# Optimization experiments

Measured on AMD Instinct MI355X. Metric: run time of the kernel, lower is better.

The kernel has to match this reference:

```python
import jax, jax.numpy as jnp
import numpy as np

B, S, F, U = 64, 512, 128, 512          # seq_length == units (required for broadcast in original code)
SIGDIM = F + F * F                       # level-2 truncated signature dimension
GRID_SIZE, SPLINE_ORDER = 5, 3           # efficient-KAN style defaults
NB = GRID_SIZE + SPLINE_ORDER            # number of b-spline basis functions per input feature
LN_EPS = 1e-3                            # keras LayerNormalization default epsilon


def _make_grid():
    h = 2.0 / GRID_SIZE  # uniform grid on [-1, 1], extended by spline order
    return -1.0 + h * jnp.arange(-SPLINE_ORDER, GRID_SIZE + SPLINE_ORDER + 1, dtype=jnp.float32)


def _b_splines(x, grid):
    # x: (N, F) -> (N, F, NB) via Cox-de Boor recursion
    x = x[..., None]
    bases = ((x >= grid[:-1]) & (x < grid[1:])).astype(x.dtype)
    for p in range(1, SPLINE_ORDER + 1):
        left = (x - grid[:-(p + 1)]) / (grid[p:-1] - grid[:-(p + 1)])
        right = (grid[p + 1:] - x) / (grid[p + 1:] - grid[1:-p])
        bases = left * bases[..., :-1] + right * bases[..., 1:]
    return bases


def _kan_linear(x, base_w, spline_w, grid):
    # KANLinear, no bias / no layernorm: silu base branch + b-spline branch
    lead = x.shape[:-1]
    base = jax.nn.silu(x) @ base_w                                  # (..., U)
    b = _b_splines(x.reshape(-1, x.shape[-1]), grid)                # (N, F, NB)
    spl = jnp.einsum('nfk,ufk->nu', b, spline_w).reshape(*lead, base_w.shape[1])
    return base + spl


def _signature2(x):
    # level-2 path signature of piecewise-linear path x: (B, S, F) -> (B, F + F*F)
    dx = x[:, 1:] - x[:, :-1]                                       # (B, S-1, F)
    s1 = dx.sum(axis=1)                                             # (B, F)
    cs = jnp.cumsum(dx, axis=1)
    prev = jnp.concatenate([jnp.zeros_like(cs[:, :1]), cs[:, :-1]], axis=1)
    s2 = jnp.einsum('bti,btj->bij', prev + 0.5 * dx, dx)            # (B, F, F)
    return jnp.concatenate([s1, s2.reshape(x.shape[0], -1)], axis=-1)


def _grkan(sig, w1, b1, w2, b2, w3, b3, w4, b4, ws, bs, gamma, beta):
    # gated residual network mapping signature -> softmax attention weights (B, U)
    h = jax.nn.elu(sig @ w1 + b1)
    h = h @ w2 + b2
    glu = jax.nn.sigmoid(h @ w3 + b3) * (h @ w4 + b4)
    y = sig @ ws + bs + glu
    mu = jnp.mean(y, axis=-1, keepdims=True)
    var = jnp.var(y, axis=-1, keepdims=True)
    y = (y - mu) / jnp.sqrt(var + LN_EPS) * gamma + beta
    return jax.nn.softmax(y, axis=-1)


def setup_inputs() -> dict:
    key = jax.random.key(0)
    ks = jax.random.split(key, 24)
    n = lambda k, shp, s=0.02: jax.random.normal(k, shp, dtype=jnp.float32) * s
    inp = {
        'inputs': jax.random.normal(ks[0], (B, S, F), dtype=jnp.float32),
        'h_prev': jax.random.normal(ks[1], (B, U), dtype=jnp.float32),
        'c_prev': jax.random.normal(ks[2], (B, U), dtype=jnp.float32),
        'time_kernel': n(ks[3], (S, 1), 0.1),
        'kan_base_w': n(ks[4], (F, U)),
        'kan_spline_w': n(ks[5], (U, F, NB)),
        'g_w1': n(ks[6], (SIGDIM, U)), 'g_b1': jnp.zeros((U,), jnp.float32),
        'g_w2': n(ks[7], (U, U)), 'g_b2': jnp.zeros((U,), jnp.float32),
        'g_w3': n(ks[8], (U, U)), 'g_b3': jnp.zeros((U,), jnp.float32),
        'g_w4': n(ks[9], (U, U)), 'g_b4': jnp.zeros((U,), jnp.float32),
        'g_skip_w': n(ks[10], (SIGDIM, U)), 'g_skip_b': jnp.zeros((U,), jnp.float32),
        'ln_gamma': jnp.ones((U,), jnp.float32), 'ln_beta': jnp.zeros((U,), jnp.float32),
        'wf': n(ks[11], (2 * U, U)), 'bf': jnp.zeros((U,), jnp.float32),
        'wi': n(ks[12], (2 * U, U)), 'bi': jnp.zeros((U,), jnp.float32),
        'wc': n(ks[13], (2 * U, U)), 'bc': jnp.zeros((U,), jnp.float32),
        'wo': n(ks[14], (2 * U, U)), 'bo': jnp.zeros((U,), jnp.float32),
    }
    return inp


def reference(inputs, h_prev, c_prev, time_kernel, kan_base_w, kan_spline_w,
              g_w1, g_b1, g_w2, g_b2, g_w3, g_b3, g_w4, g_b4, g_skip_w, g_skip_b,
              ln_gamma, ln_beta, wf, bf, wi, bi, wc, bc, wo, bo):
    grid = _make_grid()
    weighted = time_kernel * inputs                                  # (B,S,F)
    sig = _signature2(weighted)                                      # (B,SIGDIM)
    attn = _grkan(sig, g_w1, g_b1, g_w2, g_b2, g_w3, g_b3, g_w4, g_b4,
                  g_skip_w, g_skip_b, ln_gamma, ln_beta)             # (B,S) since U==S
    kan_out = _kan_linear(weighted, kan_base_w, kan_spline_w, grid)  # (B,S,U)
    attended = kan_out * attn[..., None]                             # (B,S,U)
    current = attended.mean(axis=1)                                  # (B,U)
    combined = jnp.concatenate([current, h_prev], axis=-1)           # (B,2U)
    f = jax.nn.sigmoid(combined @ wf + bf)
    i = jax.nn.sigmoid(combined @ wi + bi)
    cand = jnp.tanh(combined @ wc + bc)
    o = jax.nn.sigmoid(combined @ wo + bo)
    c_new = f * c_prev + i * cand
    h_new = o * jnp.tanh(c_new)
    return h_new, c_new
```

## Files before the change

kernel.cpp:

```cpp
#include <hip/hip_runtime.h>
#include <math.h>

#define BB 64
#define SS 512
#define FF 128
#define UU 512
#define NBB 8
#define SIGDIM (FF + FF*FF)
#define K3 16512
#define KK 1152
#define SIG_KC 43
#define SIG_STEPS 6

typedef __attribute__((ext_vector_type(8))) __bf16 bf16x8;
typedef __attribute__((ext_vector_type(8))) unsigned short u16x8;
typedef __attribute__((ext_vector_type(4))) float f32x4;

__device__ __forceinline__ unsigned short f2bf(float x) {
    unsigned int u = __float_as_uint(x);
    unsigned int r = u + 0x7FFFu + ((u >> 16) & 1u);
    return (unsigned short)(r >> 16);
}

__device__ __forceinline__ float sigmoidf(float x) { return 1.0f / (1.0f + expf(-x)); }

__global__ void k_wprep(const float* __restrict__ splw, const float* __restrict__ basew,
                        const float* __restrict__ h_prev,
                        unsigned short* __restrict__ Wt, unsigned short* __restrict__ comb_b) {
    int idx = blockIdx.x * 256 + threadIdx.x;
    if (idx >= UU * KK) return;
    int u = idx / KK, c = idx % KK;
    float v = (c < 1024) ? splw[(size_t)u * 1024 + c] : basew[(size_t)(c - 1024) * UU + u];
    Wt[idx] = f2bf(v);
    if (idx < BB * UU) {
        int b = idx >> 9, uu = idx & 511;
        comb_b[(size_t)b * 1024 + 512 + uu] = f2bf(h_prev[idx]);
    }
}

__global__ __launch_bounds__(256) void k_wt3(const float* __restrict__ w2, const float* __restrict__ w3,
                                             const float* __restrict__ w4, const float* __restrict__ wf,
                                             const float* __restrict__ wi, const float* __restrict__ wc,
                                             const float* __restrict__ wo,
                                             unsigned short* __restrict__ W2t,
                                             unsigned short* __restrict__ W3t,
                                             unsigned short* __restrict__ W4t,
                                             unsigned short* __restrict__ Wgt) {
    int kt = blockIdx.x, ut = blockIdx.y, z = blockIdx.z;
    int Kdim = (z < 3) ? 512 : 1024;
    if (kt * 64 >= Kdim) return;
    const float* src;
    unsigned short* dst;
    switch (z) {
        case 0: src = w2; dst = W2t; break;
        case 1: src = w3; dst = W3t; break;
        case 2: src = w4; dst = W4t; break;
        case 3: src = wf; dst = Wgt; break;
        case 4: src = wi; dst = Wgt + (size_t)512 * 1024; break;
        case 5: src = wc; dst = Wgt + (size_t)1024 * 1024; break;
        default: src = wo; dst = Wgt + (size_t)1536 * 1024; break;
    }
    __shared__ float tile[64][67];
    int tid = threadIdx.x;
    int k0 = kt * 64, u0 = ut * 64;
#pragma unroll
    for (int p = 0; p < 4; ++p) {
        int e = p * 256 + tid;
        int kk = e >> 4, c4 = (e & 15) * 4;
        const float4 v = *(const float4*)(src + (size_t)(k0 + kk) * UU + u0 + c4);
        tile[kk][c4 + 0] = v.x;
        tile[kk][c4 + 1] = v.y;
        tile[kk][c4 + 2] = v.z;
        tile[kk][c4 + 3] = v.w;
    }
    __syncthreads();
    int kk0 = (tid & 7) * 8;
#pragma unroll
    for (int p = 0; p < 2; ++p) {
        int uu = (tid >> 3) + p * 32;
        u16x8 ov;
#pragma unroll
        for (int j = 0; j < 8; ++j) ov[j] = f2bf(tile[kk0 + j][uu]);
        *(u16x8*)(dst + (size_t)(u0 + uu) * Kdim + k0 + kk0) = ov;
    }
}

__global__ __launch_bounds__(256) void k_adprep(const float* __restrict__ inp,
                                                const float* __restrict__ tk,
                                                unsigned short* __restrict__ aT,
                                                unsigned short* __restrict__ dT,
                                                unsigned short* __restrict__ wT) {
    int tt0 = blockIdx.x * 64, f0 = blockIdx.y * 64, b = blockIdx.z;
    __shared__ float wS[65][67];
    __shared__ float w0S[64];
    int tid = threadIdx.x;
    const float* ib = inp + (size_t)b * SS * FF;
// ... 15 lines not shown
                wS[row][c4 + 0] = 0.f;
                wS[row][c4 + 1] = 0.f;
                wS[row][c4 + 2] = 0.f;
                wS[row][c4 + 3] = 0.f;
            }
        }
    }
    __syncthreads();
    int t8 = (tid & 7) * 8;
#pragma unroll
    for (int p = 0; p < 2; ++p) {
        int ff = (tid >> 3) + p * 32;
        float w0 = w0S[ff];
        u16x8 av, dv, wv;
#pragma unroll
        for (int j = 0; j < 8; ++j) {
            int tt = t8 + j;
            float w = wS[tt][ff];
            float wn = wS[tt + 1][ff];
            bool valid = (tt0 + tt) < (SS - 1);
            float a = valid ? 0.5f * (w + wn) - w0 : 0.f;
            float d = valid ? wn - w : 0.f;
            av[j] = f2bf(a);
            dv[j] = f2bf(d);
            wv[j] = f2bf(w);
        }
        size_t o = ((size_t)b * FF + f0 + ff) * SS + tt0 + t8;
        *(u16x8*)(aT + o) = av;
        *(u16x8*)(dT + o) = dv;
        *(u16x8*)(wT + o) = wv;
    }
}

__global__ __launch_bounds__(256) void k_sig_mfma(const unsigned short* __restrict__ aT,
                                                  const unsigned short* __restrict__ dT,
                                                  float* __restrict__ s2part) {
    int kc = blockIdx.x, b = blockIdx.y;
    int tid = threadIdx.x, lane = tid & 63;
    int wv = __builtin_amdgcn_readfirstlane(tid >> 6);
    int wrow = (wv & 1) * 64, wcol = (wv >> 1) * 64;
    int k0 = kc * 128;
    const unsigned short* pa = aT + ((size_t)b * FF + wrow + (lane & 15)) * SS + k0 + (lane >> 4) * 8;
    const unsigned short* pd = dT + ((size_t)b * FF + wcol + (lane & 15)) * SS + k0 + (lane >> 4) * 8;
    f32x4 acc[4][4];
#pragma unroll
    for (int i = 0; i < 4; ++i)
#pragma unroll
        for (int j = 0; j < 4; ++j) acc[i][j] = (f32x4)(0.f);
#pragma unroll
    for (int t = 0; t < 4; ++t) {
        bf16x8 af[4], df[4];
#pragma unroll
        for (int rt = 0; rt < 4; ++rt) af[rt] = *(const bf16x8*)(pa + (size_t)rt * 16 * SS + t * 32);
#pragma unroll
        for (int ct = 0; ct < 4; ++ct) df[ct] = *(const bf16x8*)(pd + (size_t)ct * 16 * SS + t * 32);
#pragma unroll
        for (int rt = 0; rt < 4; ++rt)
#pragma unroll
            for (int ct = 0; ct < 4; ++ct)
                acc[rt][ct] = __builtin_amdgcn_mfma_f32_16x16x32_bf16(af[rt], df[ct], acc[rt][ct], 0, 0, 0);
    }
    float* outp = s2part + ((size_t)kc * BB + b) * (FF * FF);
    int quad = lane >> 4, col = lane & 15;
#pragma unroll
    for (int rt = 0; rt < 4; ++rt)
#pragma unroll
        for (int ct = 0; ct < 4; ++ct)
#pragma unroll
            for (int reg = 0; reg < 4; ++reg)
                outp[(wrow + rt * 16 + quad * 4 + reg) * FF + wcol + ct * 16 + col] = acc[rt][ct][reg];
}

__global__ void k_sig_reduce(const float* __restrict__ inp, const float* __restrict__ tk,
                             const float* __restrict__ s2part, unsigned short* __restrict__ sigb) {
    int idx = blockIdx.x * 256 + threadIdx.x;
    if (idx >= BB * SIGDIM) return;
    int b = idx / SIGDIM, r = idx % SIGDIM;
    float v;
    if (r < FF) {
        v = tk[SS - 1] * inp[((size_t)b * SS + SS - 1) * FF + r] - tk[0] * inp[(size_t)b * SS * FF + r];
    } else {
        int ij = r - FF;
        v = 0.f;
#pragma unroll
        for (int c = 0; c < 4; ++c) v += s2part[((size_t)c * BB + b) * (FF * FF) + ij];
    }
    sigb[idx] = f2bf(v);
}

__global__ __launch_bounds__(256) void k_sig_fused(const unsigned short* __restrict__ sigb,
                                                   const float* __restrict__ w1,
                                                   const float* __restrict__ gsw,
                                                   float* __restrict__ spart) {
    int nt = blockIdx.x, kc = blockIdx.y, mat = blockIdx.z;
    const float* src = mat ? gsw : w1;
    __shared__ float tile[64][67];
    int tid = threadIdx.x, lane = tid & 63;
    int wv = __builtin_amdgcn_readfirstlane(tid >> 6);
    int u0 = nt * 64;
    int n0 = wv * 16;
    int kbase = kc * (SIG_STEPS * 64);

    f32x4 acc[4];
#pragma unroll
    for (int i = 0; i < 4; ++i) acc[i] = (f32x4)(0.f);

    int nn = lane & 15;
    int kq = (lane >> 4) * 8;
    const unsigned short* pab = sigb + (size_t)nn * K3 + kq;

    for (int step = 0; step < SIG_STEPS; ++step) {
        int k0 = kbase + step * 64;
#pragma unroll
        for (int p = 0; p < 4; ++p) {
            int e = p * 256 + tid;
            int kk = e >> 4, c4 = (e & 15) * 4;
            const float4 v = *(const float4*)(src + (size_t)(k0 + kk) * UU + u0 + c4);
            tile[kk][c4 + 0] = v.x;
            tile[kk][c4 + 1] = v.y;
            tile[kk][c4 + 2] = v.z;
// ... 15 lines not shown
        }
        __syncthreads();
    }

    int col = lane & 15, quad = lane >> 4;
    float* P = spart + ((size_t)(mat * SIG_KC + kc) * 64) * UU;
#pragma unroll
    for (int rt = 0; rt < 4; ++rt)
#pragma unroll
        for (int reg = 0; reg < 4; ++reg)
            P[(size_t)(rt * 16 + quad * 4 + reg) * UU + u0 + n0 + col] = acc[rt][reg];
}

__global__ __launch_bounds__(256) void k_sig_red2(const float* __restrict__ spart,
                                                  const float* __restrict__ b1,
                                                  unsigned short* __restrict__ h1b,
                                                  float* __restrict__ skippre) {
    int idx = blockIdx.x * 256 + threadIdx.x;
    int mat = idx >> 15;
    int rem = idx & 32767;
    int m = rem >> 9, n = rem & 511;
    const float* p = spart + ((size_t)(mat * SIG_KC) * 64 + m) * UU + n;
    float v = 0.f;
#pragma unroll
    for (int kc = 0; kc < SIG_KC; ++kc) v += p[(size_t)kc * 64 * UU];
    if (mat == 0) {
        v += b1[n];
        h1b[(size_t)m * UU + n] = f2bf(v > 0.f ? v : expf(v) - 1.0f);
    } else {
        skippre[(size_t)m * UU + n] = v;
    }
}

__global__ __launch_bounds__(64) void k_h2_direct(const unsigned short* __restrict__ h1b,
                                                  const unsigned short* __restrict__ W2t,
                                                  const float* __restrict__ b2,
                                                  unsigned short* __restrict__ h2b) {
    int lane = threadIdx.x;
    int mt = blockIdx.x, nt = blockIdx.y;
    const unsigned short* pa = h1b + (size_t)(mt * 16 + (lane & 15)) * 512 + (lane >> 4) * 8;
    const unsigned short* pb = W2t + (size_t)(nt * 16 + (lane & 15)) * 512 + (lane >> 4) * 8;
    f32x4 acc0 = (f32x4)(0.f), acc1 = (f32x4)(0.f);
#pragma unroll
    for (int t = 0; t < 16; t += 2) {
        bf16x8 a0 = *(const bf16x8*)(pa + t * 32);
        bf16x8 b0 = *(const bf16x8*)(pb + t * 32);
        bf16x8 a1 = *(const bf16x8*)(pa + t * 32 + 32);
        bf16x8 b1v = *(const bf16x8*)(pb + t * 32 + 32);
        acc0 = __builtin_amdgcn_mfma_f32_16x16x32_bf16(a0, b0, acc0, 0, 0, 0);
        acc1 = __builtin_amdgcn_mfma_f32_16x16x32_bf16(a1, b1v, acc1, 0, 0, 0);
    }
    int col = lane & 15, quad = lane >> 4;
    int j = nt * 16 + col;
    float bb = b2[j];
#pragma unroll
    for (int reg = 0; reg < 4; ++reg) {
        int row = mt * 16 + quad * 4 + reg;
        h2b[(size_t)row * UU + j] = f2bf(acc0[reg] + acc1[reg] + bb);
    }
}

__global__ __launch_bounds__(64) void k_glu_direct(const unsigned short* __restrict__ h2b,
                                                   const unsigned short* __restrict__ W3t,
                                                   const unsigned short* __restrict__ W4t,
                                                   const float* __restrict__ b3,
                                                   const float* __restrict__ b4,
                                                   const float* __restrict__ skippre,
                                                   const float* __restrict__ skb,
                                                   float* __restrict__ yv) {
    int lane = threadIdx.x;
    int mt = blockIdx.x, nt = blockIdx.y;
    const unsigned short* pa = h2b + (size_t)(mt * 16 + (lane & 15)) * 512 + (lane >> 4) * 8;
    const unsigned short* pb3 = W3t + (size_t)(nt * 16 + (lane & 15)) * 512 + (lane >> 4) * 8;
    const unsigned short* pb4 = W4t + (size_t)(nt * 16 + (lane & 15)) * 512 + (lane >> 4) * 8;
    f32x4 acc3 = (f32x4)(0.f), acc4 = (f32x4)(0.f);
#pragma unroll
    for (int t = 0; t < 16; ++t) {
        bf16x8 a = *(const bf16x8*)(pa + t * 32);
        bf16x8 b3f = *(const bf16x8*)(pb3 + t * 32);
        bf16x8 b4f = *(const bf16x8*)(pb4 + t * 32);
        acc3 = __builtin_amdgcn_mfma_f32_16x16x32_bf16(a, b3f, acc3, 0, 0, 0);
        acc4 = __builtin_amdgcn_mfma_f32_16x16x32_bf16(a, b4f, acc4, 0, 0, 0);
    }
    int col = lane & 15, quad = lane >> 4;
    int j = nt * 16 + col;
    float bb3 = b3[j], bb4 = b4[j], sb = skb[j];
#pragma unroll
    for (int reg = 0; reg < 4; ++reg) {
        int row = mt * 16 + quad * 4 + reg;
        float g = sigmoidf(acc3[reg] + bb3);
        yv[(size_t)row * UU + j] = skippre[(size_t)row * UU + j] + sb + g * (acc4[reg] + bb4);
    }
}

__device__ __forceinline__ float block_sum(float v, float* red) {
    int tid = threadIdx.x;
#pragma unroll
    for (int off = 32; off > 0; off >>= 1) v += __shfl_down(v, off);
    __syncthreads();
    if ((tid & 63) == 0) red[tid >> 6] = v;
    __syncthreads();
    float r = red[0];
#pragma unroll
    for (int i = 1; i < 8; ++i) r += red[i];
    return r;
}
__device__ __forceinline__ float block_max(float v, float* red) {
    int tid = threadIdx.x;
#pragma unroll
    for (int off = 32; off > 0; off >>= 1) v = fmaxf(v, __shfl_down(v, off));
    __syncthreads();
    if ((tid & 63) == 0) red[tid >> 6] = v;
    __syncthreads();
    float r = red[0];
#pragma unroll
    for (int i = 1; i < 8; ++i) r = fmaxf(r, red[i]);
    return r;
}

__global__ void k_lnsm(const float* __restrict__ yv, const float* __restrict__ gamma,
                       const float* __restrict__ beta, float* __restrict__ attn) {
    int b = blockIdx.x, u = threadIdx.x;
    __shared__ float red[8];
    float v = yv[(size_t)b * UU + u];
    float mu = block_sum(v, red) * (1.0f / UU);
    float d = v - mu;
    float var = block_sum(d * d, red) * (1.0f / UU);
    float z = d * rsqrtf(var + 1e-3f) * gamma[u] + beta[u];
    float m = block_max(z, red);
    float e = expf(z - m);
    float Z = block_sum(e, red);
    attn[(size_t)b * UU + u] = e / Z;
}

__global__ __launch_bounds__(256) void k_kan_red(const unsigned short* __restrict__ wT,
                                                 const float* __restrict__ attn,
                                                 unsigned short* __restrict__ Aredb) {
    int b = blockIdx.x;
    int lane = threadIdx.x & 63;
    int f = blockIdx.y * 4 + (threadIdx.x >> 6);

    const u16x8 wv = *(const u16x8*)(wT + ((size_t)b * FF + f) * SS + lane * 8);
    const float* ap = attn + (size_t)b * UU + lane * 8;
    float4 a0 = *(const float4*)ap;
    float4 a1 = *(const float4*)(ap + 4);

    float acc[9] = {};
#pragma unroll
    for (int s = 0; s < 8; ++s) {
        float w = __uint_as_float((unsigned int)wv[s] << 16);
        float a = (s < 4) ? ((s == 0) ? a0.x : (s == 1) ? a0.y : (s == 2) ? a0.z : a0.w)
                          : ((s == 4) ? a1.x : (s == 5) ? a1.y : (s == 6) ? a1.z : a1.w);
        float t = (w + 2.2f) * 2.5f;
        float cf = floorf(fminf(fmaxf(t, -2.f), 13.f));
        int c = (int)cf;
        float u = t - cf;
        float u2 = u * u, u3 = u2 * u;
        float p0 = u3 * (1.f / 6.f);
        float p1 = (-3.f * u3 + 3.f * u2 + 3.f * u + 1.f) * (1.f / 6.f);
        float p2 = (3.f * u3 - 6.f * u2 + 4.f) * (1.f / 6.f);
        float onemu = 1.f - u;
        float p3 = onemu * onemu * onemu * (1.f / 6.f);
#pragma unroll
        for (int k2 = 0; k2 < 8; ++k2) {
            int d = c - k2;
            float v = (d == 0) ? p0 : (d == 1) ? p1 : (d == 2) ? p2 : (d == 3) ? p3 : 0.f;
            acc[k2] += a * v;
        }
        acc[8] += a * (w * sigmoidf(w));
    }

#pragma unroll
    for (int off = 1; off < 64; off <<= 1) {
#pragma unroll
        for (int k = 0; k < 9; ++k) acc[k] += __shfl_xor(acc[k], off);
    }

    if (lane == 0) {
        const float sc = 1.0f / SS;
        u16x8 ov;
#pragma unroll
        for (int k = 0; k < 8; ++k) ov[k] = f2bf(acc[k] * sc);
        *(u16x8*)(Aredb + (size_t)b * KK + f * 8) = ov;
        Aredb[(size_t)b * KK + 1024 + f] = f2bf(acc[8] * sc);
    }
}

__global__ __launch_bounds__(64) void k_cur_direct(const unsigned short* __restrict__ Aredb,
                                                   const unsigned short* __restrict__ Wt,
                                                   unsigned short* __restrict__ comb_b) {
    int lane = threadIdx.x;
    int mt = blockIdx.x, nt = blockIdx.y;
    const unsigned short* pa = Aredb + (size_t)(mt * 16 + (lane & 15)) * KK + (lane >> 4) * 8;
    const unsigned short* pb = Wt + (size_t)(nt * 16 + (lane & 15)) * KK + (lane >> 4) * 8;
    f32x4 acc0 = (f32x4)(0.f), acc1 = (f32x4)(0.f);
#pragma unroll 6
    for (int t = 0; t < KK / 32; t += 2) {
        bf16x8 a0 = *(const bf16x8*)(pa + t * 32);
        bf16x8 b0 = *(const bf16x8*)(pb + t * 32);
        bf16x8 a1 = *(const bf16x8*)(pa + t * 32 + 32);
        bf16x8 b1v = *(const bf16x8*)(pb + t * 32 + 32);
        acc0 = __builtin_amdgcn_mfma_f32_16x16x32_bf16(a0, b0, acc0, 0, 0, 0);
        acc1 = __builtin_amdgcn_mfma_f32_16x16x32_bf16(a1, b1v, acc1, 0, 0, 0);
    }
    int col = lane & 15, quad = lane >> 4;
    int j = nt * 16 + col;
#pragma unroll
    for (int reg = 0; reg < 4; ++reg) {
        int row = mt * 16 + quad * 4 + reg;
        comb_b[(size_t)row * 1024 + j] = f2bf(acc0[reg] + acc1[reg]);
    }
}

__global__ __launch_bounds__(64) void k_gates_direct(const unsigned short* __restrict__ comb_b,
                                                     const unsigned short* __restrict__ Wgt,
                                                     float* __restrict__ gates) {
    int lane = threadIdx.x;
    int mt = blockIdx.x, nt = blockIdx.y;
    const unsigned short* pa = comb_b + (size_t)(mt * 16 + (lane & 15)) * 1024 + (lane >> 4) * 8;
    const unsigned short* pb = Wgt + (size_t)(nt * 16 + (lane & 15)) * 1024 + (lane >> 4) * 8;
    f32x4 acc0 = (f32x4)(0.f), acc1 = (f32x4)(0.f);
#pragma unroll 8
    for (int t = 0; t < 32; t += 2) {
        bf16x8 a0 = *(const bf16x8*)(pa + t * 32);
        bf16x8 b0 = *(const bf16x8*)(pb + t * 32);
        bf16x8 a1 = *(const bf16x8*)(pa + t * 32 + 32);
        bf16x8 b1v = *(const bf16x8*)(pb + t * 32 + 32);
        acc0 = __builtin_amdgcn_mfma_f32_16x16x32_bf16(a0, b0, acc0, 0, 0, 0);
        acc1 = __builtin_amdgcn_mfma_f32_16x16x32_bf16(a1, b1v, acc1, 0, 0, 0);
    }
    int col = lane & 15, quad = lane >> 4;
    int j = nt * 16 + col;
#pragma unroll
    for (int reg = 0; reg < 4; ++reg) {
        int row = mt * 16 + quad * 4 + reg;
        gates[(size_t)row * 2048 + j] = acc0[reg] + acc1[reg];
    }
}

__global__ void k_cell(const float* __restrict__ gates,
                       const float* __restrict__ bf_, const float* __restrict__ bi_,
                       const float* __restrict__ bc_, const float* __restrict__ bo_,
                       const float* __restrict__ c_prev, float* __restrict__ out) {
    int idx = blockIdx.x * 256 + threadIdx.x;
    if (idx >= BB * UU) return;
    int b = idx >> 9, u = idx & 511;
    const float* g = gates + (size_t)b * 2048;
    float f = sigmoidf(g[u] + bf_[u]);
    float ii = sigmoidf(g[512 + u] + bi_[u]);
    float cd = tanhf(g[1024 + u] + bc_[u]);
    float o = sigmoidf(g[1536 + u] + bo_[u]);
    float cn = f * c_prev[idx] + ii * cd;
    out[idx] = o * tanhf(cn);
    out[(size_t)BB * UU + idx] = cn;
}

extern "C" void kernel_launch(void* const* d_in, const int* in_sizes, int n_in,
                              void* d_out, int out_size, void* d_ws, size_t ws_size,
                              hipStream_t stream) {
    const float* inp   = (const float*)d_in[0];
    const float* hprev = (const float*)d_in[1];
    const float* cprev = (const float*)d_in[2];
    const float* tk    = (const float*)d_in[3];
    const float* basew = (const float*)d_in[4];
    const float* splw  = (const float*)d_in[5];
    const float* gw1   = (const float*)d_in[6];
    const float* gb1   = (const float*)d_in[7];
    const float* gw2   = (const float*)d_in[8];
    const float* gb2   = (const float*)d_in[9];
    const float* gw3   = (const float*)d_in[10];
    const float* gb3   = (const float*)d_in[11];
    const float* gw4   = (const float*)d_in[12];
    const float* gb4   = (const float*)d_in[13];
    const float* gsw   = (const float*)d_in[14];
    const float* gsb   = (const float*)d_in[15];
    const float* lng   = (const float*)d_in[16];
    const float* lnb   = (const float*)d_in[17];
    const float* wf    = (const float*)d_in[18];
    const float* bf_   = (const float*)d_in[19];
    const float* wi    = (const float*)d_in[20];
    const float* bi_   = (const float*)d_in[21];
    const float* wc    = (const float*)d_in[22];
    const float* bc_   = (const float*)d_in[23];
    const float* wo    = (const float*)d_in[24];
    const float* bo_   = (const float*)d_in[25];
    float* out = (float*)d_out;

    float* ws = (float*)d_ws;
    size_t o = 0;
    unsigned short* Wt  = (unsigned short*)(ws + o); o += (size_t)UU * KK / 2;
    float* s2part   = ws + o; o += (size_t)4 * BB * FF * FF;
    unsigned short* aT = (unsigned short*)(ws + o); o += (size_t)BB * FF * SS / 2;
    unsigned short* dT = (unsigned short*)(ws + o); o += (size_t)BB * FF * SS / 2;
    unsigned short* wT = (unsigned short*)(ws + o); o += (size_t)BB * FF * SS / 2;
    unsigned short* sigb = (unsigned short*)(ws + o); o += (size_t)BB * K3 / 2;
    float* spart    = ws + o; o += (size_t)2 * SIG_KC * 64 * UU;
    float* skippre  = ws + o; o += (size_t)BB * UU;
    unsigned short* h1b = (unsigned short*)(ws + o); o += (size_t)BB * UU / 2;
    unsigned short* h2b = (unsigned short*)(ws + o); o += (size_t)BB * UU / 2;
    float* yv       = ws + o; o += (size_t)BB * UU;
    float* attn     = ws + o; o += (size_t)BB * UU;
    unsigned short* Aredb = (unsigned short*)(ws + o); o += (size_t)BB * KK / 2;
    unsigned short* W2t = (unsigned short*)(ws + o); o += (size_t)512 * 512 / 2;
    unsigned short* W3t = (unsigned short*)(ws + o); o += (size_t)512 * 512 / 2;
    unsigned short* W4t = (unsigned short*)(ws + o); o += (size_t)512 * 512 / 2;
    unsigned short* Wgt = (unsigned short*)(ws + o); o += (size_t)2048 * 1024 / 2;
    unsigned short* comb_b = (unsigned short*)(ws + o); o += (size_t)BB * 1024 / 2;
    float* gates    = ws + o; o += (size_t)BB * 2048;
    (void)ws_size; (void)in_sizes; (void)n_in; (void)out_size;

    k_wprep<<<(UU * KK + 255) / 256, 256, 0, stream>>>(splw, basew, hprev, Wt, comb_b);
    k_wt3<<<dim3(16, 8, 7), 256, 0, stream>>>(gw2, gw3, gw4, wf, wi, wc, wo, W2t, W3t, W4t, Wgt);
    k_adprep<<<dim3(8, 2, BB), 256, 0, stream>>>(inp, tk, aT, dT, wT);
    k_sig_mfma<<<dim3(4, BB), 256, 0, stream>>>(aT, dT, s2part);
    k_sig_reduce<<<(BB * SIGDIM + 255) / 256, 256, 0, stream>>>(inp, tk, s2part, sigb);
    k_sig_fused<<<dim3(8, SIG_KC, 2), 256, 0, stream>>>(sigb, gw1, gsw, spart);
    k_sig_red2<<<256, 256, 0, stream>>>(spart, gb1, h1b, skippre);
    k_h2_direct<<<dim3(4, 32), 64, 0, stream>>>(h1b, W2t, gb2, h2b);
    k_glu_direct<<<dim3(4, 32), 64, 0, stream>>>(h2b, W3t, W4t, gb3, gb4, skippre, gsb, yv);
    k_lnsm<<<BB, UU, 0, stream>>>(yv, lng, lnb, attn);
    k_kan_red<<<dim3(BB, FF / 4), 256, 0, stream>>>(wT, attn, Aredb);
    k_cur_direct<<<dim3(4, 32), 64, 0, stream>>>(Aredb, Wt, comb_b);
    k_gates_direct<<<dim3(4, 128), 64, 0, stream>>>(comb_b, Wgt, gates);
    k_cell<<<(BB * UU + 255) / 256, 256, 0, stream>>>(gates, bf_, bi_, bc_, bo_, cprev, out);
}
```

Before: 252.1 us.

## Fuse weight prep, signature reduce, GRN+LN+softmax, and cur+gates kernels

Merges the two weight-conversion kernels into one launch, and makes the level-2 signature MFMA kernel cover the full sequence per batch so the separate split-K reduce pass goes away. The h2/GLU/LayerNorm/softmax chain becomes one kernel, and so do the current and gates GEMMs, with intermediates kept in shared memory. The goal is to cut kernel launches and global round trips for the small intermediates. In exchange, the fused GEMMs run on only 4 blocks and the signature kernel on 64 blocks, so far less of the GPU is used in parallel.

```diff
diff --git a/kernel.cpp b/kernel.cpp
--- a/kernel.cpp
+++ b/kernel.cpp
@@ -5,7 +5,6 @@
 #define SS 512
 #define FF 128
 #define UU 512
-#define NBB 8
 #define SIGDIM (FF + FF*FF)
 #define K3 16512
 #define KK 1152
@@ -24,34 +23,35 @@
 
 __device__ __forceinline__ float sigmoidf(float x) { return 1.0f / (1.0f + expf(-x)); }
 
-__global__ void k_wprep(const float* __restrict__ splw, const float* __restrict__ basew,
-                        const float* __restrict__ h_prev,
-                        unsigned short* __restrict__ Wt, unsigned short* __restrict__ comb_b) {
-    int idx = blockIdx.x * 256 + threadIdx.x;
-    if (idx >= UU * KK) return;
-    int u = idx / KK, c = idx % KK;
-    float v = (c < 1024) ? splw[(size_t)u * 1024 + c] : basew[(size_t)(c - 1024) * UU + u];
-    Wt[idx] = f2bf(v);
-    if (idx < BB * UU) {
-        int b = idx >> 9, uu = idx & 511;
-        comb_b[(size_t)b * 1024 + 512 + uu] = f2bf(h_prev[idx]);
-    }
-}
-
-__global__ __launch_bounds__(256) void k_wt3(const float* __restrict__ w2, const float* __restrict__ w3,
-                                             const float* __restrict__ w4, const float* __restrict__ wf,
-                                             const float* __restrict__ wi, const float* __restrict__ wc,
-                                             const float* __restrict__ wo,
-                                             unsigned short* __restrict__ W2t,
-                                             unsigned short* __restrict__ W3t,
-                                             unsigned short* __restrict__ W4t,
-                                             unsigned short* __restrict__ Wgt) {
-    int kt = blockIdx.x, ut = blockIdx.y, z = blockIdx.z;
-    int Kdim = (z < 3) ? 512 : 1024;
+__global__ __launch_bounds__(256) void k_prep(const float* __restrict__ splw,
+                                              const float* __restrict__ basew,
+                                              const float* __restrict__ w2, const float* __restrict__ w3,
+                                              const float* __restrict__ w4, const float* __restrict__ wf,
+                                              const float* __restrict__ wi, const float* __restrict__ wc,
+                                              const float* __restrict__ wo,
+                                              unsigned short* __restrict__ Wt,
+                                              unsigned short* __restrict__ W2t,
+                                              unsigned short* __restrict__ W3t,
+                                              unsigned short* __restrict__ W4t,
+                                              unsigned short* __restrict__ Wgt) {
+    int z = blockIdx.z;
+    int tid = threadIdx.x;
+    if (z == 0) {
+        int base = (blockIdx.y * 16 + blockIdx.x) * 256 + tid;
+        for (int idx = base; idx < UU * KK; idx += 128 * 256) {
+            int u = idx / KK, c = idx % KK;
+            float v = (c < 1024) ? splw[(size_t)u * 1024 + c] : basew[(size_t)(c - 1024) * UU + u];
+            Wt[idx] = f2bf(v);
+        }
+        return;
+    }
+    int zz = z - 1;
+    int Kdim = (zz < 3) ? 512 : 1024;
+    int kt = blockIdx.x, ut = blockIdx.y;
     if (kt * 64 >= Kdim) return;
     const float* src;
     unsigned short* dst;
-    switch (z) {
+    switch (zz) {
         case 0: src = w2; dst = W2t; break;
         case 1: src = w3; dst = W3t; break;
         case 2: src = w4; dst = W4t; break;
@@ -61,7 +61,6 @@
         default: src = wo; dst = Wgt + (size_t)1536 * 1024; break;
     }
     __shared__ float tile[64][67];
-    int tid = threadIdx.x;
     int k0 = kt * 64, u0 = ut * 64;
 #pragma unroll
     for (int p = 0; p < 4; ++p) {
@@ -143,23 +142,23 @@
     }
 }
 
-__global__ __launch_bounds__(256) void k_sig_mfma(const unsigned short* __restrict__ aT,
-                                                  const unsigned short* __restrict__ dT,
-                                                  float* __restrict__ s2part) {
-    int kc = blockIdx.x, b = blockIdx.y;
+__global__ __launch_bounds__(256) void k_sig2(const unsigned short* __restrict__ aT,
+                                              const unsigned short* __restrict__ dT,
+                                              const float* __restrict__ inp,
+                                              const float* __restrict__ tk,
+                                              unsigned short* __restrict__ sigb) {
+    int b = blockIdx.x;
     int tid = threadIdx.x, lane = tid & 63;
     int wv = __builtin_amdgcn_readfirstlane(tid >> 6);
     int wrow = (wv & 1) * 64, wcol = (wv >> 1) * 64;
-    int k0 = kc * 128;
-    const unsigned short* pa = aT + ((size_t)b * FF + wrow + (lane & 15)) * SS + k0 + (lane >> 4) * 8;
-    const unsigned short* pd = dT + ((size_t)b * FF + wcol + (lane & 15)) * SS + k0 + (lane >> 4) * 8;
+    const unsigned short* pa = aT + ((size_t)b * FF + wrow + (lane & 15)) * SS + (lane >> 4) * 8;
+    const unsigned short* pd = dT + ((size_t)b * FF + wcol + (lane & 15)) * SS + (lane >> 4) * 8;
     f32x4 acc[4][4];
 #pragma unroll
     for (int i = 0; i < 4; ++i)
 #pragma unroll
         for (int j = 0; j < 4; ++j) acc[i][j] = (f32x4)(0.f);
-#pragma unroll
-    for (int t = 0; t < 4; ++t) {
+    for (int t = 0; t < 16; ++t) {
         bf16x8 af[4], df[4];
 #pragma unroll
         for (int rt = 0; rt < 4; ++rt) af[rt] = *(const bf16x8*)(pa + (size_t)rt * 16 * SS + t * 32);
@@ -171,7 +170,11 @@
             for (int ct = 0; ct < 4; ++ct)
                 acc[rt][ct] = __builtin_amdgcn_mfma_f32_16x16x32_bf16(af[rt], df[ct], acc[rt][ct], 0, 0, 0);
     }
-    float* outp = s2part + ((size_t)kc * BB + b) * (FF * FF);
+    unsigned short* ob = sigb + (size_t)b * SIGDIM;
+    if (tid < FF) {
+        float v = tk[SS - 1] * inp[((size_t)b * SS + SS - 1) * FF + tid] - tk[0] * inp[(size_t)b * SS * FF + tid];
+        ob[tid] = f2bf(v);
+    }
     int quad = lane >> 4, col = lane & 15;
 #pragma unroll
     for (int rt = 0; rt < 4; ++rt)
@@ -179,24 +182,7 @@
         for (int ct = 0; ct < 4; ++ct)
 #pragma unroll
             for (int reg = 0; reg < 4; ++reg)
-                outp[(wrow + rt * 16 + quad * 4 + reg) * FF + wcol + ct * 16 + col] = acc[rt][ct][reg];
-}
-
-__global__ void k_sig_reduce(const float* __restrict__ inp, const float* __restrict__ tk,
-                             const float* __restrict__ s2part, unsigned short* __restrict__ sigb) {
-    int idx = blockIdx.x * 256 + threadIdx.x;
-    if (idx >= BB * SIGDIM) return;
-    int b = idx / SIGDIM, r = idx % SIGDIM;
-    float v;
-    if (r < FF) {
-        v = tk[SS - 1] * inp[((size_t)b * SS + SS - 1) * FF + r] - tk[0] * inp[(size_t)b * SS * FF + r];
-    } else {
-        int ij = r - FF;
-        v = 0.f;
-#pragma unroll
-        for (int c = 0; c < 4; ++c) v += s2part[((size_t)c * BB + b) * (FF * FF) + ij];
-    }
-    sigb[idx] = f2bf(v);
+                ob[FF + (wrow + rt * 16 + quad * 4 + reg) * FF + wcol + ct * 16 + col] = f2bf(acc[rt][ct][reg]);
 }
 
 __global__ __launch_bounds__(256) void k_sig_fused(const unsigned short* __restrict__ sigb,
@@ -278,105 +264,117 @@
     }
 }
 
-__global__ __launch_bounds__(64) void k_h2_direct(const unsigned short* __restrict__ h1b,
-                                                  const unsigned short* __restrict__ W2t,
-                                                  const float* __restrict__ b2,
-                                                  unsigned short* __restrict__ h2b) {
-    int lane = threadIdx.x;
-    int mt = blockIdx.x, nt = blockIdx.y;
-    const unsigned short* pa = h1b + (size_t)(mt * 16 + (lane & 15)) * 512 + (lane >> 4) * 8;
-    const unsigned short* pb = W2t + (size_t)(nt * 16 + (lane & 15)) * 512 + (lane >> 4) * 8;
-    f32x4 acc0 = (f32x4)(0.f), acc1 = (f32x4)(0.f);
-#pragma unroll
-    for (int t = 0; t < 16; t += 2) {
-        bf16x8 a0 = *(const bf16x8*)(pa + t * 32);
-        bf16x8 b0 = *(const bf16x8*)(pb + t * 32);
-        bf16x8 a1 = *(const bf16x8*)(pa + t * 32 + 32);
-        bf16x8 b1v = *(const bf16x8*)(pb + t * 32 + 32);
-        acc0 = __builtin_amdgcn_mfma_f32_16x16x32_bf16(a0, b0, acc0, 0, 0, 0);
-        acc1 = __builtin_amdgcn_mfma_f32_16x16x32_bf16(a1, b1v, acc1, 0, 0, 0);
-    }
-    int col = lane & 15, quad = lane >> 4;
-    int j = nt * 16 + col;
-    float bb = b2[j];
-#pragma unroll
-    for (int reg = 0; reg < 4; ++reg) {
-        int row = mt * 16 + quad * 4 + reg;
-        h2b[(size_t)row * UU + j] = f2bf(acc0[reg] + acc1[reg] + bb);
-    }
-}
-
-__global__ __launch_bounds__(64) void k_glu_direct(const unsigned short* __restrict__ h2b,
-                                                   const unsigned short* __restrict__ W3t,
-                                                   const unsigned short* __restrict__ W4t,
-                                                   const float* __restrict__ b3,
-                                                   const float* __restrict__ b4,
-                                                   const float* __restrict__ skippre,
-                                                   const float* __restrict__ skb,
-                                                   float* __restrict__ yv) {
-    int lane = threadIdx.x;
-    int mt = blockIdx.x, nt = blockIdx.y;
-    const unsigned short* pa = h2b + (size_t)(mt * 16 + (lane & 15)) * 512 + (lane >> 4) * 8;
-    const unsigned short* pb3 = W3t + (size_t)(nt * 16 + (lane & 15)) * 512 + (lane >> 4) * 8;
-    const unsigned short* pb4 = W4t + (size_t)(nt * 16 + (lane & 15)) * 512 + (lane >> 4) * 8;
-    f32x4 acc3 = (f32x4)(0.f), acc4 = (f32x4)(0.f);
-#pragma unroll
-    for (int t = 0; t < 16; ++t) {
-        bf16x8 a = *(const bf16x8*)(pa + t * 32);
-        bf16x8 b3f = *(const bf16x8*)(pb3 + t * 32);
-        bf16x8 b4f = *(const bf16x8*)(pb4 + t * 32);
-        acc3 = __builtin_amdgcn_mfma_f32_16x16x32_bf16(a, b3f, acc3, 0, 0, 0);
-        acc4 = __builtin_amdgcn_mfma_f32_16x16x32_bf16(a, b4f, acc4, 0, 0, 0);
-    }
-    int col = lane & 15, quad = lane >> 4;
-    int j = nt * 16 + col;
-    float bb3 = b3[j], bb4 = b4[j], sb = skb[j];
-#pragma unroll
-    for (int reg = 0; reg < 4; ++reg) {
-        int row = mt * 16 + quad * 4 + reg;
-        float g = sigmoidf(acc3[reg] + bb3);
-        yv[(size_t)row * UU + j] = skippre[(size_t)row * UU + j] + sb + g * (acc4[reg] + bb4);
-    }
-}
-
-__device__ __forceinline__ float block_sum(float v, float* red) {
-    int tid = threadIdx.x;
-#pragma unroll
-    for (int off = 32; off > 0; off >>= 1) v += __shfl_down(v, off);
+__global__ __launch_bounds__(512) void k_grn(const unsigned short* __restrict__ h1b,
+                                             const float* __restrict__ skippre,
+                                             const unsigned short* __restrict__ W2t,
+                                             const float* __restrict__ b2,
+                                             const unsigned short* __restrict__ W3t,
+                                             const unsigned short* __restrict__ W4t,
+                                             const float* __restrict__ b3,
+                                             const float* __restrict__ b4,
+                                             const float* __restrict__ skb,
+                                             const float* __restrict__ gamma,
+                                             const float* __restrict__ beta,
+                                             float* __restrict__ attn) {
+    int bq = blockIdx.x;
+    int m0 = bq * 16;
+    __shared__ unsigned short h2S[16][520];
+    __shared__ float yS[16][516];
+    int tid = threadIdx.x, lane = tid & 63;
+    int wv = tid >> 6;
+    int n0 = wv * 64;
+    int col = lane & 15, quad = lane >> 4, kq = quad * 8;
+
+    {
+        f32x4 acc[4];
+#pragma unroll
+        for (int i = 0; i < 4; ++i) acc[i] = (f32x4)(0.f);
+        const unsigned short* pa = h1b + (size_t)(m0 + col) * UU + kq;
+#pragma unroll
+        for (int t = 0; t < 16; ++t) {
+            bf16x8 af = *(const bf16x8*)(pa + t * 32);
+#pragma unroll
+            for (int nt2 = 0; nt2 < 4; ++nt2) {
+                bf16x8 bf = *(const bf16x8*)(W2t + (size_t)(n0 + nt2 * 16 + col) * 512 + t * 32 + kq);
+                acc[nt2] = __builtin_amdgcn_mfma_f32_16x16x32_bf16(af, bf, acc[nt2], 0, 0, 0);
+            }
+        }
+#pragma unroll
+        for (int nt2 = 0; nt2 < 4; ++nt2) {
+            int j = n0 + nt2 * 16 + col;
+            float bb = b2[j];
+#pragma unroll
+            for (int reg = 0; reg < 4; ++reg)
+                h2S[quad * 4 + reg][j] = f2bf(acc[nt2][reg] + bb);
+        }
+    }
     __syncthreads();
-    if ((tid & 63) == 0) red[tid >> 6] = v;
+    {
+        f32x4 a3[4], a4[4];
+#pragma unroll
+        for (int i = 0; i < 4; ++i) { a3[i] = (f32x4)(0.f); a4[i] = (f32x4)(0.f); }
+#pragma unroll
+        for (int t = 0; t < 16; ++t) {
+            bf16x8 af = *(const bf16x8*)&h2S[col][t * 32 + kq];
+#pragma unroll
+            for (int nt2 = 0; nt2 < 4; ++nt2) {
+                bf16x8 b3f = *(const bf16x8*)(W3t + (size_t)(n0 + nt2 * 16 + col) * 512 + t * 32 + kq);
+                bf16x8 b4f = *(const bf16x8*)(W4t + (size_t)(n0 + nt2 * 16 + col) * 512 + t * 32 + kq);
+                a3[nt2] = __builtin_amdgcn_mfma_f32_16x16x32_bf16(af, b3f, a3[nt2], 0, 0, 0);
+                a4[nt2] = __builtin_amdgcn_mfma_f32_16x16x32_bf16(af, b4f, a4[nt2], 0, 0, 0);
+            }
+        }
+#pragma unroll
+        for (int nt2 = 0; nt2 < 4; ++nt2) {
+            int j = n0 + nt2 * 16 + col;
+            float bb3 = b3[j], bb4 = b4[j], sb = skb[j];
+#pragma unroll
+            for (int reg = 0; reg < 4; ++reg) {
+                int row = quad * 4 + reg;
+                float g = sigmoidf(a3[nt2][reg] + bb3);
+                yS[row][j] = skippre[(size_t)(m0 + row) * UU + j] + sb + g * (a4[nt2][reg] + bb4);
+            }
+        }
+    }
     __syncthreads();
-    float r = red[0];
-#pragma unroll
-    for (int i = 1; i < 8; ++i) r += red[i];
-    return r;
-}
-__device__ __forceinline__ float block_max(float v, float* red) {
-    int tid = threadIdx.x;
-#pragma unroll
-    for (int off = 32; off > 0; off >>= 1) v = fmaxf(v, __shfl_down(v, off));
-    __syncthreads();
-    if ((tid & 63) == 0) red[tid >> 6] = v;
-    __syncthreads();
-    float r = red[0];
-#pragma unroll
-    for (int i = 1; i < 8; ++i) r = fmaxf(r, red[i]);
-    return r;
-}
-
-__global__ void k_lnsm(const float* __restrict__ yv, const float* __restrict__ gamma,
-                       const float* __restrict__ beta, float* __restrict__ attn) {
-    int b = blockIdx.x, u = threadIdx.x;
-    __shared__ float red[8];
-    float v = yv[(size_t)b * UU + u];
-    float mu = block_sum(v, red) * (1.0f / UU);
-    float d = v - mu;
-    float var = block_sum(d * d, red) * (1.0f / UU);
-    float z = d * rsqrtf(var + 1e-3f) * gamma[u] + beta[u];
-    float m = block_max(z, red);
-    float e = expf(z - m);
-    float Z = block_sum(e, red);
-    attn[(size_t)b * UU + u] = e / Z;
+#pragma unroll
+    for (int r = 0; r < 2; ++r) {
+        int m = wv * 2 + r;
+        int c0 = lane * 8;
+        float v[8];
+#pragma unroll
+        for (int i = 0; i < 8; ++i) v[i] = yS[m][c0 + i];
+        float s = 0.f;
+#pragma unroll
+        for (int i = 0; i < 8; ++i) s += v[i];
+#pragma unroll
+        for (int off = 1; off < 64; off <<= 1) s += __shfl_xor(s, off);
+        float mu = s * (1.0f / UU);
+        float q = 0.f;
+#pragma unroll
+        for (int i = 0; i < 8; ++i) { float d = v[i] - mu; q += d * d; }
+#pragma unroll
+        for (int off = 1; off < 64; off <<= 1) q += __shfl_xor(q, off);
+        float rstd = rsqrtf(q * (1.0f / UU) + 1e-3f);
+        float z[8];
+        float mx = -3.4e38f;
+#pragma unroll
+        for (int i = 0; i < 8; ++i) {
+            z[i] = (v[i] - mu) * rstd * gamma[c0 + i] + beta[c0 + i];
+            mx = fmaxf(mx, z[i]);
+        }
+#pragma unroll
+        for (int off = 1; off < 64; off <<= 1) mx = fmaxf(mx, __shfl_xor(mx, off));
+        float es = 0.f;
+#pragma unroll
+        for (int i = 0; i < 8; ++i) { z[i] = expf(z[i] - mx); es += z[i]; }
+#pragma unroll
+        for (int off = 1; off < 64; off <<= 1) es += __shfl_xor(es, off);
+        float inv = 1.0f / es;
+        float* op = attn + (size_t)(m0 + m) * UU + c0;
+#pragma unroll
+        for (int i = 0; i < 8; ++i) op[i] = z[i] * inv;
+    }
 }
 
 __global__ __launch_bounds__(256) void k_kan_red(const unsigned short* __restrict__ wT,
@@ -432,55 +430,67 @@
     }
 }
 
-__global__ __launch_bounds__(64) void k_cur_direct(const unsigned short* __restrict__ Aredb,
-                                                   const unsigned short* __restrict__ Wt,
-                                                   unsigned short* __restrict__ comb_b) {
-    int lane = threadIdx.x;
-    int mt = blockIdx.x, nt = blockIdx.y;
-    const unsigned short* pa = Aredb + (size_t)(mt * 16 + (lane & 15)) * KK + (lane >> 4) * 8;
-    const unsigned short* pb = Wt + (size_t)(nt * 16 + (lane & 15)) * KK + (lane >> 4) * 8;
-    f32x4 acc0 = (f32x4)(0.f), acc1 = (f32x4)(0.f);
-#pragma unroll 6
-    for (int t = 0; t < KK / 32; t += 2) {
-        bf16x8 a0 = *(const bf16x8*)(pa + t * 32);
-        bf16x8 b0 = *(const bf16x8*)(pb + t * 32);
-        bf16x8 a1 = *(const bf16x8*)(pa + t * 32 + 32);
-        bf16x8 b1v = *(const bf16x8*)(pb + t * 32 + 32);
-        acc0 = __builtin_amdgcn_mfma_f32_16x16x32_bf16(a0, b0, acc0, 0, 0, 0);
-        acc1 = __builtin_amdgcn_mfma_f32_16x16x32_bf16(a1, b1v, acc1, 0, 0, 0);
-    }
-    int col = lane & 15, quad = lane >> 4;
-    int j = nt * 16 + col;
-#pragma unroll
-    for (int reg = 0; reg < 4; ++reg) {
-        int row = mt * 16 + quad * 4 + reg;
-        comb_b[(size_t)row * 1024 + j] = f2bf(acc0[reg] + acc1[reg]);
-    }
-}
-
-__global__ __launch_bounds__(64) void k_gates_direct(const unsigned short* __restrict__ comb_b,
-                                                     const unsigned short* __restrict__ Wgt,
-                                                     float* __restrict__ gates) {
-    int lane = threadIdx.x;
-    int mt = blockIdx.x, nt = blockIdx.y;
-    const unsigned short* pa = comb_b + (size_t)(mt * 16 + (lane & 15)) * 1024 + (lane >> 4) * 8;
-    const unsigned short* pb = Wgt + (size_t)(nt * 16 + (lane & 15)) * 1024 + (lane >> 4) * 8;
-    f32x4 acc0 = (f32x4)(0.f), acc1 = (f32x4)(0.f);
-#pragma unroll 8
-    for (int t = 0; t < 32; t += 2) {
-        bf16x8 a0 = *(const bf16x8*)(pa + t * 32);
-        bf16x8 b0 = *(const bf16x8*)(pb + t * 32);
-        bf16x8 a1 = *(const bf16x8*)(pa + t * 32 + 32);
-        bf16x8 b1v = *(const bf16x8*)(pb + t * 32 + 32);
-        acc0 = __builtin_amdgcn_mfma_f32_16x16x32_bf16(a0, b0, acc0, 0, 0, 0);
-        acc1 = __builtin_amdgcn_mfma_f32_16x16x32_bf16(a1, b1v, acc1, 0, 0, 0);
-    }
-    int col = lane & 15, quad = lane >> 4;
-    int j = nt * 16 + col;
-#pragma unroll
-    for (int reg = 0; reg < 4; ++reg) {
-        int row = mt * 16 + quad * 4 + reg;
-        gates[(size_t)row * 2048 + j] = acc0[reg] + acc1[reg];
+__global__ __launch_bounds__(512) void k_curgates(const unsigned short* __restrict__ Aredb,
+                                                  const unsigned short* __restrict__ Wt,
+                                                  const float* __restrict__ h_prev,
+                                                  const unsigned short* __restrict__ Wgt,
+                                                  float* __restrict__ gates) {
+    int bq = blockIdx.x;
+    int m0 = bq * 16;
+    __shared__ unsigned short combS[16][1048];
+    int tid = threadIdx.x, lane = tid & 63;
+    int wv = tid >> 6;
+    int col = lane & 15, quad = lane >> 4, kq = quad * 8;
+
+    {
+        int n0 = wv * 64;
+        f32x4 acc[4];
+#pragma unroll
+        for (int i = 0; i < 4; ++i) acc[i] = (f32x4)(0.f);
+        const unsigned short* pa = Aredb + (size_t)(m0 + col) * KK + kq;
+#pragma unroll 4
+        for (int t = 0; t < 36; ++t) {
+            bf16x8 af = *(const bf16x8*)(pa + t * 32);
+#pragma unroll
+            for (int nt2 = 0; nt2 < 4; ++nt2) {
+                bf16x8 bf = *(const bf16x8*)(Wt + (size_t)(n0 + nt2 * 16 + col) * KK + t * 32 + kq);
+                acc[nt2] = __builtin_amdgcn_mfma_f32_16x16x32_bf16(af, bf, acc[nt2], 0, 0, 0);
+            }
+        }
+#pragma unroll
+        for (int nt2 = 0; nt2 < 4; ++nt2) {
+            int j = n0 + nt2 * 16 + col;
+#pragma unroll
+            for (int reg = 0; reg < 4; ++reg)
+                combS[quad * 4 + reg][j] = f2bf(acc[nt2][reg]);
+        }
+    }
+    for (int e = tid; e < 16 * 512; e += 512) {
+        int m = e >> 9, u = e & 511;
+        combS[m][512 + u] = f2bf(h_prev[(size_t)(m0 + m) * UU + u]);
+    }
+    __syncthreads();
+    {
+        int ng0 = wv * 256;
+        f32x4 acc[16];
+#pragma unroll
+        for (int i = 0; i < 16; ++i) acc[i] = (f32x4)(0.f);
+#pragma unroll 2
+        for (int t = 0; t < 32; ++t) {
+            bf16x8 af = *(const bf16x8*)&combS[col][t * 32 + kq];
+#pragma unroll
+            for (int nt8 = 0; nt8 < 16; ++nt8) {
+                bf16x8 bf = *(const bf16x8*)(Wgt + (size_t)(ng0 + nt8 * 16 + col) * 1024 + t * 32 + kq);
+                acc[nt8] = __builtin_amdgcn_mfma_f32_16x16x32_bf16(af, bf, acc[nt8], 0, 0, 0);
+            }
+        }
+#pragma unroll
+        for (int nt8 = 0; nt8 < 16; ++nt8) {
+            int j = ng0 + nt8 * 16 + col;
+#pragma unroll
+            for (int reg = 0; reg < 4; ++reg)
+                gates[(size_t)(m0 + quad * 4 + reg) * 2048 + j] = acc[nt8][reg];
+        }
     }
 }
 
@@ -535,7 +545,6 @@
     float* ws = (float*)d_ws;
     size_t o = 0;
     unsigned short* Wt  = (unsigned short*)(ws + o); o += (size_t)UU * KK / 2;
-    float* s2part   = ws + o; o += (size_t)4 * BB * FF * FF;
     unsigned short* aT = (unsigned short*)(ws + o); o += (size_t)BB * FF * SS / 2;
     unsigned short* dT = (unsigned short*)(ws + o); o += (size_t)BB * FF * SS / 2;
     unsigned short* wT = (unsigned short*)(ws + o); o += (size_t)BB * FF * SS / 2;
@@ -543,30 +552,23 @@
     float* spart    = ws + o; o += (size_t)2 * SIG_KC * 64 * UU;
     float* skippre  = ws + o; o += (size_t)BB * UU;
     unsigned short* h1b = (unsigned short*)(ws + o); o += (size_t)BB * UU / 2;
-    unsigned short* h2b = (unsigned short*)(ws + o); o += (size_t)BB * UU / 2;
-    float* yv       = ws + o; o += (size_t)BB * UU;
     float* attn     = ws + o; o += (size_t)BB * UU;
     unsigned short* Aredb = (unsigned short*)(ws + o); o += (size_t)BB * KK / 2;
     unsigned short* W2t = (unsigned short*)(ws + o); o += (size_t)512 * 512 / 2;
     unsigned short* W3t = (unsigned short*)(ws + o); o += (size_t)512 * 512 / 2;
     unsigned short* W4t = (unsigned short*)(ws + o); o += (size_t)512 * 512 / 2;
     unsigned short* Wgt = (unsigned short*)(ws + o); o += (size_t)2048 * 1024 / 2;
-    unsigned short* comb_b = (unsigned short*)(ws + o); o += (size_t)BB * 1024 / 2;
     float* gates    = ws + o; o += (size_t)BB * 2048;
     (void)ws_size; (void)in_sizes; (void)n_in; (void)out_size;
 
-    k_wprep<<<(UU * KK + 255) / 256, 256, 0, stream>>>(splw, basew, hprev, Wt, comb_b);
-    k_wt3<<<dim3(16, 8, 7), 256, 0, stream>>>(gw2, gw3, gw4, wf, wi, wc, wo, W2t, W3t, W4t, Wgt);
+    k_prep<<<dim3(16, 8, 8), 256, 0, stream>>>(splw, basew, gw2, gw3, gw4, wf, wi, wc, wo,
+                                               Wt, W2t, W3t, W4t, Wgt);
     k_adprep<<<dim3(8, 2, BB), 256, 0, stream>>>(inp, tk, aT, dT, wT);
-    k_sig_mfma<<<dim3(4, BB), 256, 0, stream>>>(aT, dT, s2part);
-    k_sig_reduce<<<(BB * SIGDIM + 255) / 256, 256, 0, stream>>>(inp, tk, s2part, sigb);
+    k_sig2<<<BB, 256, 0, stream>>>(aT, dT, inp, tk, sigb);
     k_sig_fused<<<dim3(8, SIG_KC, 2), 256, 0, stream>>>(sigb, gw1, gsw, spart);
     k_sig_red2<<<256, 256, 0, stream>>>(spart, gb1, h1b, skippre);
-    k_h2_direct<<<dim3(4, 32), 64, 0, stream>>>(h1b, W2t, gb2, h2b);
-    k_glu_direct<<<dim3(4, 32), 64, 0, stream>>>(h2b, W3t, W4t, gb3, gb4, skippre, gsb, yv);
-    k_lnsm<<<BB, UU, 0, stream>>>(yv, lng, lnb, attn);
+    k_grn<<<4, 512, 0, stream>>>(h1b, skippre, W2t, gb2, W3t, W4t, gb3, gb4, gsb, lng, lnb, attn);
     k_kan_red<<<dim3(BB, FF / 4), 256, 0, stream>>>(wT, attn, Aredb);
-    k_cur_direct<<<dim3(4, 32), 64, 0, stream>>>(Aredb, Wt, comb_b);
-    k_gates_direct<<<dim3(4, 128), 64, 0, stream>>>(comb_b, Wgt, gates);
+    k_curgates<<<4, 512, 0, stream>>>(Aredb, Wt, hprev, Wgt, gates);
     k_cell<<<(BB * UU + 255) / 256, 256, 0, stream>>>(gates, bf_, bi_, bc_, bo_, cprev, out);
 }
```

Result: slower. 473.8 us (+88.0%).

## Merge weight-prep kernels and fold signature reduction into single-pass MFMA kernel

Applied to the files above, without the earlier changes.

Two weight-conversion kernels become one launch with a z-slice that grid-strides over the KAN weight transpose. The level-2 signature MFMA kernel now runs the full 512-step reduction per batch in one block and writes bf16 results straight into the signature buffer, level-1 terms included. This removes the fp32 partial-sum buffer and the separate reduce kernel. The cost is fewer blocks (64 instead of 256) for the signature GEMM, so each block runs a longer serial K loop at lower parallelism.

```diff
diff --git a/kernel.cpp b/kernel.cpp
--- a/kernel.cpp
+++ b/kernel.cpp
@@ -5,7 +5,6 @@
 #define SS 512
 #define FF 128
 #define UU 512
-#define NBB 8
 #define SIGDIM (FF + FF*FF)
 #define K3 16512
 #define KK 1152
@@ -24,34 +23,41 @@
 
 __device__ __forceinline__ float sigmoidf(float x) { return 1.0f / (1.0f + expf(-x)); }
 
-__global__ void k_wprep(const float* __restrict__ splw, const float* __restrict__ basew,
-                        const float* __restrict__ h_prev,
-                        unsigned short* __restrict__ Wt, unsigned short* __restrict__ comb_b) {
-    int idx = blockIdx.x * 256 + threadIdx.x;
-    if (idx >= UU * KK) return;
-    int u = idx / KK, c = idx % KK;
-    float v = (c < 1024) ? splw[(size_t)u * 1024 + c] : basew[(size_t)(c - 1024) * UU + u];
-    Wt[idx] = f2bf(v);
-    if (idx < BB * UU) {
-        int b = idx >> 9, uu = idx & 511;
-        comb_b[(size_t)b * 1024 + 512 + uu] = f2bf(h_prev[idx]);
-    }
-}
-
-__global__ __launch_bounds__(256) void k_wt3(const float* __restrict__ w2, const float* __restrict__ w3,
-                                             const float* __restrict__ w4, const float* __restrict__ wf,
-                                             const float* __restrict__ wi, const float* __restrict__ wc,
-                                             const float* __restrict__ wo,
-                                             unsigned short* __restrict__ W2t,
-                                             unsigned short* __restrict__ W3t,
-                                             unsigned short* __restrict__ W4t,
-                                             unsigned short* __restrict__ Wgt) {
-    int kt = blockIdx.x, ut = blockIdx.y, z = blockIdx.z;
-    int Kdim = (z < 3) ? 512 : 1024;
+__global__ __launch_bounds__(256) void k_prep(const float* __restrict__ splw,
+                                              const float* __restrict__ basew,
+                                              const float* __restrict__ h_prev,
+                                              const float* __restrict__ w2, const float* __restrict__ w3,
+                                              const float* __restrict__ w4, const float* __restrict__ wf,
+                                              const float* __restrict__ wi, const float* __restrict__ wc,
+                                              const float* __restrict__ wo,
+                                              unsigned short* __restrict__ Wt,
+                                              unsigned short* __restrict__ comb_b,
+                                              unsigned short* __restrict__ W2t,
+                                              unsigned short* __restrict__ W3t,
+                                              unsigned short* __restrict__ W4t,
+                                              unsigned short* __restrict__ Wgt) {
+    int z = blockIdx.z;
+    int tid = threadIdx.x;
+    if (z == 0) {
+        int base = (blockIdx.y * 16 + blockIdx.x) * 256 + tid;
+        {
+            int b = base >> 9, uu = base & 511;
+            comb_b[(size_t)b * 1024 + 512 + uu] = f2bf(h_prev[base]);
+        }
+        for (int idx = base; idx < UU * KK; idx += 128 * 256) {
+            int u = idx / KK, c = idx % KK;
+            float v = (c < 1024) ? splw[(size_t)u * 1024 + c] : basew[(size_t)(c - 1024) * UU + u];
+            Wt[idx] = f2bf(v);
+        }
+        return;
+    }
+    int zz = z - 1;
+    int Kdim = (zz < 3) ? 512 : 1024;
+    int kt = blockIdx.x, ut = blockIdx.y;
     if (kt * 64 >= Kdim) return;
     const float* src;
     unsigned short* dst;
-    switch (z) {
+    switch (zz) {
         case 0: src = w2; dst = W2t; break;
         case 1: src = w3; dst = W3t; break;
         case 2: src = w4; dst = W4t; break;
@@ -61,7 +67,6 @@
         default: src = wo; dst = Wgt + (size_t)1536 * 1024; break;
     }
     __shared__ float tile[64][67];
-    int tid = threadIdx.x;
     int k0 = kt * 64, u0 = ut * 64;
 #pragma unroll
     for (int p = 0; p < 4; ++p) {
@@ -143,23 +148,23 @@
     }
 }
 
-__global__ __launch_bounds__(256) void k_sig_mfma(const unsigned short* __restrict__ aT,
-                                                  const unsigned short* __restrict__ dT,
-                                                  float* __restrict__ s2part) {
-    int kc = blockIdx.x, b = blockIdx.y;
+__global__ __launch_bounds__(256) void k_sig2(const unsigned short* __restrict__ aT,
+                                              const unsigned short* __restrict__ dT,
+                                              const float* __restrict__ inp,
+                                              const float* __restrict__ tk,
+                                              unsigned short* __restrict__ sigb) {
+    int b = blockIdx.x;
     int tid = threadIdx.x, lane = tid & 63;
     int wv = __builtin_amdgcn_readfirstlane(tid >> 6);
     int wrow = (wv & 1) * 64, wcol = (wv >> 1) * 64;
-    int k0 = kc * 128;
-    const unsigned short* pa = aT + ((size_t)b * FF + wrow + (lane & 15)) * SS + k0 + (lane >> 4) * 8;
-    const unsigned short* pd = dT + ((size_t)b * FF + wcol + (lane & 15)) * SS + k0 + (lane >> 4) * 8;
+    const unsigned short* pa = aT + ((size_t)b * FF + wrow + (lane & 15)) * SS + (lane >> 4) * 8;
+    const unsigned short* pd = dT + ((size_t)b * FF + wcol + (lane & 15)) * SS + (lane >> 4) * 8;
     f32x4 acc[4][4];
 #pragma unroll
     for (int i = 0; i < 4; ++i)
 #pragma unroll
         for (int j = 0; j < 4; ++j) acc[i][j] = (f32x4)(0.f);
-#pragma unroll
-    for (int t = 0; t < 4; ++t) {
+    for (int t = 0; t < 16; ++t) {
         bf16x8 af[4], df[4];
 #pragma unroll
         for (int rt = 0; rt < 4; ++rt) af[rt] = *(const bf16x8*)(pa + (size_t)rt * 16 * SS + t * 32);
@@ -171,7 +176,11 @@
             for (int ct = 0; ct < 4; ++ct)
                 acc[rt][ct] = __builtin_amdgcn_mfma_f32_16x16x32_bf16(af[rt], df[ct], acc[rt][ct], 0, 0, 0);
     }
-    float* outp = s2part + ((size_t)kc * BB + b) * (FF * FF);
+    unsigned short* ob = sigb + (size_t)b * SIGDIM;
+    if (tid < FF) {
+        float v = tk[SS - 1] * inp[((size_t)b * SS + SS - 1) * FF + tid] - tk[0] * inp[(size_t)b * SS * FF + tid];
+        ob[tid] = f2bf(v);
+    }
     int quad = lane >> 4, col = lane & 15;
 #pragma unroll
     for (int rt = 0; rt < 4; ++rt)
@@ -179,24 +188,7 @@
         for (int ct = 0; ct < 4; ++ct)
 #pragma unroll
             for (int reg = 0; reg < 4; ++reg)
-                outp[(wrow + rt * 16 + quad * 4 + reg) * FF + wcol + ct * 16 + col] = acc[rt][ct][reg];
-}
-
-__global__ void k_sig_reduce(const float* __restrict__ inp, const float* __restrict__ tk,
-                             const float* __restrict__ s2part, unsigned short* __restrict__ sigb) {
-    int idx = blockIdx.x * 256 + threadIdx.x;
-    if (idx >= BB * SIGDIM) return;
-    int b = idx / SIGDIM, r = idx % SIGDIM;
-    float v;
-    if (r < FF) {
-        v = tk[SS - 1] * inp[((size_t)b * SS + SS - 1) * FF + r] - tk[0] * inp[(size_t)b * SS * FF + r];
-    } else {
-        int ij = r - FF;
-        v = 0.f;
-#pragma unroll
-        for (int c = 0; c < 4; ++c) v += s2part[((size_t)c * BB + b) * (FF * FF) + ij];
-    }
-    sigb[idx] = f2bf(v);
+                ob[FF + (wrow + rt * 16 + quad * 4 + reg) * FF + wcol + ct * 16 + col] = f2bf(acc[rt][ct][reg]);
 }
 
 __global__ __launch_bounds__(256) void k_sig_fused(const unsigned short* __restrict__ sigb,
@@ -535,7 +527,6 @@
     float* ws = (float*)d_ws;
     size_t o = 0;
     unsigned short* Wt  = (unsigned short*)(ws + o); o += (size_t)UU * KK / 2;
-    float* s2part   = ws + o; o += (size_t)4 * BB * FF * FF;
     unsigned short* aT = (unsigned short*)(ws + o); o += (size_t)BB * FF * SS / 2;
     unsigned short* dT = (unsigned short*)(ws + o); o += (size_t)BB * FF * SS / 2;
     unsigned short* wT = (unsigned short*)(ws + o); o += (size_t)BB * FF * SS / 2;
@@ -555,11 +546,10 @@
     float* gates    = ws + o; o += (size_t)BB * 2048;
     (void)ws_size; (void)in_sizes; (void)n_in; (void)out_size;
 
-    k_wprep<<<(UU * KK + 255) / 256, 256, 0, stream>>>(splw, basew, hprev, Wt, comb_b);
-    k_wt3<<<dim3(16, 8, 7), 256, 0, stream>>>(gw2, gw3, gw4, wf, wi, wc, wo, W2t, W3t, W4t, Wgt);
+    k_prep<<<dim3(16, 8, 8), 256, 0, stream>>>(splw, basew, hprev, gw2, gw3, gw4, wf, wi, wc, wo,
+                                               Wt, comb_b, W2t, W3t, W4t, Wgt);
     k_adprep<<<dim3(8, 2, BB), 256, 0, stream>>>(inp, tk, aT, dT, wT);
-    k_sig_mfma<<<dim3(4, BB), 256, 0, stream>>>(aT, dT, s2part);
-    k_sig_reduce<<<(BB * SIGDIM + 255) / 256, 256, 0, stream>>>(inp, tk, s2part, sigb);
+    k_sig2<<<BB, 256, 0, stream>>>(aT, dT, inp, tk, sigb);
     k_sig_fused<<<dim3(8, SIG_KC, 2), 256, 0, stream>>>(sigb, gw1, gsw, spart);
     k_sig_red2<<<256, 256, 0, stream>>>(spart, gb1, h1b, skippre);
     k_h2_direct<<<dim3(4, 32), 64, 0, stream>>>(h1b, W2t, gb2, h2b);
```

New measurement: 255.9 us. Within noise of the previous version (+1.5%).
